# Performance work log

Measured on AMD Instinct MI355X. Metric: run time of the kernel, lower is better.

The kernel has to match this reference:

```python
import jax, jax.numpy as jnp
import numpy as np
from jax import lax

ANGRES = 5


def _conv(x, w, stride=(1, 1), pad=((1, 1), (1, 1)), dil=(1, 1)):
    return lax.conv_general_dilated(x, w, stride, pad, rhs_dilation=dil,
                                    dimension_numbers=('NCHW', 'OIHW', 'NCHW'))


def _lrelu(x):
    return jnp.where(x >= 0, x, 0.1 * x)


def _block_s(x, w):
    # SAI input: split into 5x5 grid of (sh,sw) views, conv each view, emit MacPI-interleaved layout
    B, C, H, W = x.shape
    sh, sw = H // 5, W // 5
    p = x.reshape(B, C, 5, sh, 5, sw).transpose(0, 2, 4, 1, 3, 5).reshape(B * 25, C, sh, sw)
    y = _conv(p, w).reshape(B, 5, 5, C, sh, sw)
    # (B,bi,bj,C,sh,sw) -> (B,C,sh,bi,sw,bj) -> (B,C,H,W)   [torch permute(0,3,4,1,5,2)]
    return y.transpose(0, 3, 4, 1, 5, 2).reshape(B, C, H, W)


def _block_a(x, w):
    # MacPI input: conv each 5x5 macropixel independently (zero pad at block edges)
    B, C, H, W = x.shape
    nh, nw = H // 5, W // 5
    p = x.reshape(B, C, nh, 5, nw, 5).transpose(0, 2, 4, 1, 3, 5).reshape(B * nh * nw, C, 5, 5)
    y = _conv(p, w)
    return y.reshape(B, nh, nw, C, 5, 5).transpose(0, 3, 1, 4, 2, 5).reshape(B, C, H, W)


def _epi(x, w1, w2, a):
    # EPI conv: [1,3a] kernel, stride [1,a], pad [0,a]; then 1x1 to a*C; then 1D pixel shuffle on W
    y = _lrelu(_conv(x, w1, stride=(1, a), pad=((0, 0), (a, a))))
    y = _lrelu(_conv(y, w2, pad=((0, 0), (0, 0))))
    B, aC, H, Wa = y.shape
    C = aC // a
    return y.reshape(B, a, C, H, Wa).transpose(0, 2, 3, 4, 1).reshape(B, C, H, Wa * a)


def _att_fuse(buf, alpha, gamma, beta, eps=1e-5):
    # covariance-based GLU attention over the N=4 branches
    B, NC, H, W = buf.shape
    N = 4
    C = NC // N
    x5 = buf.reshape(B, N, C, H, W)
    xr = x5.reshape(B, N, C * H * W)
    M = xr.shape[-1]
    xc = xr - jnp.mean(xr, axis=-1, keepdims=True)
    cov = jnp.einsum('bnm,bkm->bnk', xc, xc) * (alpha / (M - 1))  # [B,N,N]
    norm = cov / jnp.sqrt(jnp.mean(cov * cov, axis=(1, 2), keepdims=True) + eps)
    g = gamma * norm + beta
    att = g * jax.nn.sigmoid(g)  # GLU of duplicated halves
    out = jnp.einsum('bnk,bkm->bnm', att, xr).reshape(B, N, C, H, W) + x5
    return out.reshape(B, NC, H, W)


def _mac2sai(x, a):
    B, C, HU, WV = x.shape
    h, w = HU // a, WV // a
    return x.reshape(B, C, a, h, a, w).transpose(0, 1, 3, 5, 2, 4).reshape(B, C, h * a, w * a)


def _tsfefb(x, x1, ws, wa, we1, we2, al, ga, be, wf1, wf2, a):
    feaSpa = _lrelu(_block_s(x1, ws))
    feaAng = _lrelu(_block_a(x, wa))
    feaH = _epi(x, we1, we2, a)
    feaV = jnp.transpose(_epi(jnp.transpose(x, (0, 1, 3, 2)), we1, we2, a), (0, 1, 3, 2))
    buf = jnp.concatenate([feaSpa, feaAng, feaH, feaV], axis=1)
    out = _att_fuse(buf, al, ga, be)
    y = _lrelu(_conv(out, wf1, pad=((0, 0), (0, 0))))
    y = _conv(y, wf2, pad=((a, a), (a, a)), dil=(a, a))
    return y + x


def setup_inputs() -> dict:
    key = jax.random.key(0)
    ks = jax.random.split(key, 12)
    B, C, a, n = 4, 64, ANGRES, 4
    H = W = a * 32  # 160

    def w(k, shape):
        fan_in = float(np.prod(shape[2:]))
        return jax.random.normal(k, shape, jnp.float32) / np.float32(np.sqrt(fan_in))

    return {
        'x': jax.random.normal(ks[0], (B, C, H, W), jnp.float32),
        'x1': jax.random.normal(ks[1], (B, C, H, W), jnp.float32),
        'w_spa': w(ks[2], (n, C, C, 3, 3)),
        'w_ang': w(ks[3], (n, C, C, 3, 3)),
        'w_epi1': w(ks[4], (n, C, C, 1, 3 * a)),
        'w_epi2': w(ks[5], (n, a * C, C, 1, 1)),
        'alpha': jnp.ones((n,), jnp.float32),
        'gamma': 0.1 * jax.random.normal(ks[6], (n,), jnp.float32),
        'beta': 0.1 * jax.random.normal(ks[7], (n,), jnp.float32),
        'w_fuse1': w(ks[8], (n, C, 4 * C, 1, 1)),
        'w_fuse2': w(ks[9], (n, C, C, 3, 3)),
    }


def reference(x, x1, w_spa, w_ang, w_epi1, w_epi2, alpha, gamma, beta, w_fuse1, w_fuse2):
    a = ANGRES
    buf, buf1 = x, x1
    for i in range(w_spa.shape[0]):
        buf = _tsfefb(buf, buf1, w_spa[i], w_ang[i], w_epi1[i], w_epi2[i],
                      alpha[i], gamma[i], beta[i], w_fuse1[i], w_fuse2[i], a)
        buf1 = _mac2sai(buf, a)
    return buf
```

## Files before the change

### kernel.cpp

```cpp
#include <hip/hip_runtime.h>

__device__ __forceinline__ float lrelu(float v){ return v >= 0.f ? v : 0.1f*v; }


__global__ __launch_bounds__(256) void k_spa(const float* __restrict__ buf1, const float* __restrict__ w,
                                             float* __restrict__ out){
  const int b = blockIdx.x / 50, r2 = blockIdx.x % 50;
  const int view = r2 >> 1, half = r2 & 1;
  const int bi = view / 5, bj = view % 5;
  const int th0 = half*16;
  const int cog = blockIdx.y;
  const int tid = threadIdx.x;
  __shared__ float plane[2][18*38];
  for (int idx=tid; idx<2*18*38; idx+=256) ((float*)plane)[idx]=0.f;
  float acc[2][8];
  #pragma unroll
  for (int k=0;k<2;k++)
    #pragma unroll
    for (int c=0;c<8;c++) acc[k][c]=0.f;
  const float* src = buf1 + (size_t)b*1638400 + bi*32*160 + bj*32;
  const float* wb = w + (size_t)(cog*8)*576;
  const int sr = tid >> 3, sq = (tid & 7)*4;
  const int vr = th0 - 1 + sr;
  const bool rowok = (tid < 144) && ((unsigned)vr < 32u);
  __syncthreads();
  if (rowok)
    *(float4*)&plane[0][sr*38 + 4 + sq] = *(const float4*)(src + vr*160 + sq);
  __syncthreads();
  const int lr = tid >> 5, c = tid & 31;
  for (int ci=0; ci<64; ci++){
    float4 nx;
    const bool ld = rowok && (ci < 63);
    if (ld) nx = *(const float4*)(src + (size_t)(ci+1)*25600 + vr*160 + sq);
    const float* P = plane[ci & 1];
    float t0[9], t1[9];
    {
      const float* pp = &P[lr*38 + c + 3];
      t0[0]=pp[0];  t0[1]=pp[1];  t0[2]=pp[2];
      t0[3]=pp[38]; t0[4]=pp[39]; t0[5]=pp[40];
      t0[6]=pp[76]; t0[7]=pp[77]; t0[8]=pp[78];
      const float* qq = pp + 8*38;
      t1[0]=qq[0];  t1[1]=qq[1];  t1[2]=qq[2];
      t1[3]=qq[38]; t1[4]=qq[39]; t1[5]=qq[40];
      t1[6]=qq[76]; t1[7]=qq[77]; t1[8]=qq[78];
    }
    #pragma unroll
    for (int co=0;co<8;co++){
      const float* wp = wb + (size_t)co*576 + ci*9;
      float w0=wp[0],w1=wp[1],w2=wp[2],w3=wp[3],w4=wp[4],w5=wp[5],w6=wp[6],w7=wp[7],w8=wp[8];
      acc[0][co] += t0[0]*w0+t0[1]*w1+t0[2]*w2+t0[3]*w3+t0[4]*w4
                  + t0[5]*w5+t0[6]*w6+t0[7]*w7+t0[8]*w8;
      acc[1][co] += t1[0]*w0+t1[1]*w1+t1[2]*w2+t1[3]*w3+t1[4]*w4
                  + t1[5]*w5+t1[6]*w6+t1[7]*w7+t1[8]*w8;
    }
    if (ld) *(float4*)&plane[(ci+1)&1][sr*38 + 4 + sq] = nx;
    __syncthreads();
  }
  #pragma unroll
  for (int k=0;k<2;k++){
    int si = th0 + lr + k*8;
    int h = si*5 + bi, wq = c*5 + bj;
    #pragma unroll
    for (int co=0;co<8;co++){
      int ch = b*64 + cog*8 + co;
      out[(size_t)ch*25600 + h*160 + wq] = lrelu(acc[k][co]);
    }
  }
}

__global__ __launch_bounds__(320) void k_ang(const float* __restrict__ bufA, const float* __restrict__ w,
                                             float* __restrict__ out){
  const int b = blockIdx.x >> 4, mip = blockIdx.x & 15;
  const int cog = blockIdx.y;
  const int tid = threadIdx.x;
  __shared__ float lds[2][2240];
  for (int i=tid; i<2*2240; i+=320) ((float*)lds)[i] = 0.f;

  const int u = tid >> 6, mi_l = (tid >> 5) & 1, mp = tid & 31;
  int offm[3], offa[3];
  #pragma unroll
  for (int du=0; du<3; du++){
    offm[du] = mi_l*896 + (u+du)*128 + mp*4;
    offa[du] = 1792 + mi_l*224 + (u+du)*32 + mp;
  }
  const bool st1 = tid < 80;
  int sdst0[4], sdst1[4];
  const int rr0 = tid/40,       q0 = tid%40;
  const int rr1 = (tid+320)/40, q1 = (tid+320)%40;
  #pragma unroll
  for (int j=0;j<4;j++){
    int g = q0*4+j, mpw = g/5, vw = g - mpw*5;
    int miw = rr0/5, uw = rr0 - miw*5;
    sdst0[j] = (vw<4) ? (miw*896 + (1+uw)*128 + mpw*4 + vw)
                      : (1792 + miw*224 + (1+uw)*32 + mpw);
    g = q1*4+j; mpw = g/5; vw = g - mpw*5;
    miw = rr1/5; uw = rr1 - miw*5;
    sdst1[j] = (vw<4) ? (miw*896 + (1+uw)*128 + mpw*4 + vw)
                      : (1792 + miw*224 + (1+uw)*32 + mpw);
  }
  const float* src = bufA + (size_t)b*1638400 + (size_t)(mip*10)*160;
  const float* wb = w + (size_t)(cog*4)*576;

  float acc[4][5];
  #pragma unroll
  for (int co=0;co<4;co++)
    #pragma unroll
    for (int v=0;v<5;v++) acc[co][v]=0.f;

  __syncthreads();
  {
    float4 x0 = *(const float4*)(src + rr0*160 + q0*4);
    lds[0][sdst0[0]]=x0.x; lds[0][sdst0[1]]=x0.y; lds[0][sdst0[2]]=x0.z; lds[0][sdst0[3]]=x0.w;
    if (st1){
      float4 x1 = *(const float4*)(src + rr1*160 + q1*4);
      lds[0][sdst1[0]]=x1.x; lds[0][sdst1[1]]=x1.y; lds[0][sdst1[2]]=x1.z; lds[0][sdst1[3]]=x1.w;
    }
  }
  __syncthreads();
  for (int ci=0; ci<64; ci++){
    float4 n0, n1;
    if (ci < 63){
      n0 = *(const float4*)(src + (size_t)(ci+1)*25600 + rr0*160 + q0*4);
      if (st1) n1 = *(const float4*)(src + (size_t)(ci+1)*25600 + rr1*160 + q1*4);
    }
    const float* P = lds[ci & 1];
    float c[3][5];
    #pragma unroll
    for (int du=0;du<3;du++){
      float4 m = *(const float4*)&P[offm[du]];
      c[du][0]=m.x; c[du][1]=m.y; c[du][2]=m.z; c[du][3]=m.w;
      c[du][4]=P[offa[du]];
    }
    #pragma unroll
    for (int co=0;co<4;co++){
      const float* wp = wb + (size_t)co*576 + ci*9;
      float w0=wp[0],w1=wp[1],w2=wp[2],w3=wp[3],w4=wp[4],w5=wp[5],w6=wp[6],w7=wp[7],w8=wp[8];
      acc[co][0] += c[0][0]*w1 + c[0][1]*w2
                  + c[1][0]*w4 + c[1][1]*w5
                  + c[2][0]*w7 + c[2][1]*w8;
      acc[co][1] += c[0][0]*w0 + c[0][1]*w1 + c[0][2]*w2
                  + c[1][0]*w3 + c[1][1]*w4 + c[1][2]*w5
                  + c[2][0]*w6 + c[2][1]*w7 + c[2][2]*w8;
      acc[co][2] += c[0][1]*w0 + c[0][2]*w1 + c[0][3]*w2
                  + c[1][1]*w3 + c[1][2]*w4 + c[1][3]*w5
                  + c[2][1]*w6 + c[2][2]*w7 + c[2][3]*w8;
      acc[co][3] += c[0][2]*w0 + c[0][3]*w1 + c[0][4]*w2
                  + c[1][2]*w3 + c[1][3]*w4 + c[1][4]*w5
                  + c[2][2]*w6 + c[2][3]*w7 + c[2][4]*w8;
      acc[co][4] += c[0][3]*w0 + c[0][4]*w1
                  + c[1][3]*w3 + c[1][4]*w4
                  + c[2][3]*w6 + c[2][4]*w7;
    }
    if (ci < 63){
      float* Q = lds[(ci+1)&1];
      Q[sdst0[0]]=n0.x; Q[sdst0[1]]=n0.y; Q[sdst0[2]]=n0.z; Q[sdst0[3]]=n0.w;
      if (st1){ Q[sdst1[0]]=n1.x; Q[sdst1[1]]=n1.y; Q[sdst1[2]]=n1.z; Q[sdst1[3]]=n1.w; }
    }
    __syncthreads();
  }
  const int h = (mip*2 + mi_l)*5 + u;
  const int wc0 = mp*5;
  #pragma unroll
  for (int co=0;co<4;co++){
    int ch = b*64 + cog*4 + co;
    float* op = out + (size_t)ch*25600 + (size_t)h*160 + wc0;
    op[0]=lrelu(acc[co][0]); op[1]=lrelu(acc[co][1]); op[2]=lrelu(acc[co][2]);
    op[3]=lrelu(acc[co][3]); op[4]=lrelu(acc[co][4]);
  }
}

template<int VERT>
__global__ __launch_bounds__(320) void k_epi(const float* __restrict__ bufA, const float* __restrict__ we1,
                                             const float* __restrict__ we2, float* __restrict__ out){
  const int b = blockIdx.x / 160, hw = blockIdx.x % 160;
  const int tid = threadIdx.x;
  __shared__ float rowp[64*176];
  __shared__ float y1s[64*32];
  if (VERT){
    for (int idx=tid; idx<10240; idx+=320){
      int ci = idx/160, x = idx - ci*160;
      rowp[ci*176 + 8 + x] = bufA[(size_t)b*1638400 + (size_t)ci*25600 + (size_t)x*160 + hw];
    }
  } else {
    for (int ft=tid; ft<2560; ft+=320){
      int ci = ft/40, xq = (ft - ci*40)*4;
      *(float4*)&rowp[ci*176 + 8 + xq] =
        *(const float4*)(bufA + (size_t)b*1638400 + (size_t)ci*25600 + (size_t)hw*160 + xq);
    }
  }
  for (int idx=tid; idx<64*16; idx+=320){
    int ci = idx>>4, j = idx&15;
    rowp[ci*176 + (j<8 ? j : 160+j)] = 0.f;
  }
  __syncthreads();
  if (tid < 256){
    const int co = tid >> 2, wv0 = (tid & 3)*8;
    const int a0 = 2 + wv0*5;
    float acc[8];
    #pragma unroll
    for (int j=0;j<8;j++) acc[j]=0.f;
    const float* wp0 = we1 + (size_t)co*960;
    for (int ci=0; ci<64; ci++){
      float fl[52];
      const float* rp = &rowp[ci*176 + a0];
      #pragma unroll
      for (int m=0;m<26;m++) *(float2*)&fl[2*m] = *(const float2*)&rp[2*m];
      const float* wp = wp0 + ci*15;
      #pragma unroll
      for (int t=0;t<15;t++){
        float wt = wp[t];
        #pragma unroll
        for (int j=0;j<8;j++) acc[j] += fl[1 + j*5 + t]*wt;
      }
    }
    #pragma unroll
    for (int j=0;j<8;j++) y1s[co*32 + wv0 + j] = lrelu(acc[j]);
  }
  __syncthreads();
  {
    const int oc = tid, kk = oc >> 6, c = oc & 63;
    float a2[32];
    #pragma unroll
    for (int wv=0;wv<32;wv++) a2[wv]=0.f;
    const float* wp = we2 + (size_t)oc*64;
    for (int ci=0; ci<64; ci++){
      float wt = wp[ci];
      const float* yp = &y1s[ci*32];
      #pragma unroll
      for (int wv=0; wv<32; wv++) a2[wv] += yp[wv]*wt;
    }
    float* y2s = rowp;
    #pragma unroll
    for (int wv=0; wv<32; wv++) y2s[c*160 + wv*5 + kk] = lrelu(a2[wv]);
  }
  __syncthreads();
  {
    const float* y2s = rowp;
    for (int k=0;k<8;k++){
      int f = (tid + k*320)*4;
      int c = f/160, rr = f - c*160;
      *(float4*)(out + (size_t)(b*64+c)*25600 + (size_t)hw*160 + rr) = *(const float4*)&y2s[c*160+rr];
    }
  }
}

__global__ __launch_bounds__(256) void k_permV(const float* __restrict__ tmp, float* __restrict__ dst){
  const int bc = blockIdx.x;
  const int ti = blockIdx.y / 5, tj = blockIdx.y % 5;
  const int hw0 = ti*32, r0 = tj*32;
  const int lx = threadIdx.x & 31, ly = threadIdx.x >> 5;
  __shared__ float tile[32][33];
  const float* in = tmp + (size_t)bc*25600;
  float* outp = dst + (size_t)bc*25600;
  for (int yy=ly; yy<32; yy+=8)
    tile[yy][lx] = in[(size_t)(hw0+yy)*160 + r0 + lx];
  __syncthreads();
  for (int yy=ly; yy<32; yy+=8)
    outp[(size_t)(r0+yy)*160 + hw0 + lx] = tile[lx][yy];
}

__global__ __launch_bounds__(256) void k_permM(const float* __restrict__ A, float* __restrict__ dst){
  const int bc = blockIdx.x >> 5, hh = blockIdx.x & 31;
  const int tid = threadIdx.x;
  __shared__ float rows[5*160];
  const float* in = A + (size_t)bc*25600;
  if (tid < 200){
    int ai = tid/40, q = (tid - ai*40)*4;
    *(float4*)&rows[ai*160 + q] = *(const float4*)(in + (size_t)(ai*32+hh)*160 + q);
  }
  __syncthreads();
  float* outp = dst + (size_t)bc*25600 + (size_t)hh*800;
  for (int t=tid; t<800; t+=256){
    int ww = t/25, r2 = t - ww*25, ai = r2/5, aj = r2 - ai*5;
    outp[t] = rows[ai*160 + aj*32 + ww];
  }
}

__global__ __launch_bounds__(256) void k_red(const float* __restrict__ b0, const float* __restrict__ b1,
                                             const float* __restrict__ b2, const float* __restrict__ b3,
                                             float* __restrict__ part){
  const int b = blockIdx.y, blk = blockIdx.x;
  const int tid = threadIdx.x;
  const size_t off = (size_t)b*1638400 + (size_t)blk*25600;
  float s0=0,s1=0,s2=0,s3=0;
  float p00=0,p01=0,p02=0,p03=0,p11=0,p12=0,p13=0,p22=0,p23=0,p33=0;
  for (int it=0; it<25; it++){
    size_t m = off + it*1024 + tid*4;
    float4 x0 = *(const float4*)(b0+m);
    float4 x1 = *(const float4*)(b1+m);
    float4 x2 = *(const float4*)(b2+m);
    float4 x3 = *(const float4*)(b3+m);
    s0 += (x0.x+x0.y)+(x0.z+x0.w);
    s1 += (x1.x+x1.y)+(x1.z+x1.w);
    s2 += (x2.x+x2.y)+(x2.z+x2.w);
    s3 += (x3.x+x3.y)+(x3.z+x3.w);
    p00 += x0.x*x0.x+x0.y*x0.y+x0.z*x0.z+x0.w*x0.w;
    p01 += x0.x*x1.x+x0.y*x1.y+x0.z*x1.z+x0.w*x1.w;
    p02 += x0.x*x2.x+x0.y*x2.y+x0.z*x2.z+x0.w*x2.w;
    p03 += x0.x*x3.x+x0.y*x3.y+x0.z*x3.z+x0.w*x3.w;
    p11 += x1.x*x1.x+x1.y*x1.y+x1.z*x1.z+x1.w*x1.w;
    p12 += x1.x*x2.x+x1.y*x2.y+x1.z*x2.z+x1.w*x2.w;
    p13 += x1.x*x3.x+x1.y*x3.y+x1.z*x3.z+x1.w*x3.w;
    p22 += x2.x*x2.x+x2.y*x2.y+x2.z*x2.z+x2.w*x2.w;
    p23 += x2.x*x3.x+x2.y*x3.y+x2.z*x3.z+x2.w*x3.w;
    p33 += x3.x*x3.x+x3.y*x3.y+x3.z*x3.z+x3.w*x3.w;
  }
  float vals[14] = {s0,s1,s2,s3,p00,p01,p02,p03,p11,p12,p13,p22,p23,p33};
  __shared__ float red[4][14];
  int lane = tid & 63, wv = tid >> 6;
  #pragma unroll
  for (int j=0;j<14;j++){
    float v = vals[j];
    #pragma unroll
    for (int o=32;o>0;o>>=1) v += __shfl_down(v,o,64);
    if (lane==0) red[wv][j]=v;
  }
  __syncthreads();
  if (tid<14) part[((size_t)b*64+blk)*16 + tid] = red[0][tid]+red[1][tid]+red[2][tid]+red[3][tid];
}

__global__ __launch_bounds__(256) void k_attW(const float* __restrict__ part,
        const float* __restrict__ alpha, const float* __restrict__ gamma, const float* __restrict__ beta,
        int iblk, const float* __restrict__ wf1, float* __restrict__ Weff){
  const int b = blockIdx.x, tid = threadIdx.x;
  __shared__ float st[14];
  __shared__ float att[16];
  if (tid<14){
    float t=0;
    for (int blk=0;blk<64;blk++) t += part[((size_t)b*64+blk)*16 + tid];
    st[tid]=t;
  }
  __syncthreads();
  if (tid==0){
    const float M = 1638400.f;
    float s[4] = {st[0],st[1],st[2],st[3]};
    float S[4][4];
    S[0][0]=st[4];  S[0][1]=S[1][0]=st[5];  S[0][2]=S[2][0]=st[6];  S[0][3]=S[3][0]=st[7];
    S[1][1]=st[8];  S[1][2]=S[2][1]=st[9];  S[1][3]=S[3][1]=st[10];
    S[2][2]=st[11]; S[2][3]=S[3][2]=st[12]; S[3][3]=st[13];
    float al=alpha[iblk], ga=gamma[iblk], be=beta[iblk];
    float scale = al/(M-1.f);
    float cov[4][4], ss=0.f;
    for (int n=0;n<4;n++) for (int k=0;k<4;k++){
      float c = (S[n][k] - s[n]*s[k]/M)*scale;
      cov[n][k]=c; ss += c*c;
    }
    float rms = sqrtf(ss/16.f + 1e-5f);
    for (int n=0;n<4;n++) for (int k=0;k<4;k++){
      float g = ga*cov[n][k]/rms + be;
      att[n*4+k] = g/(1.f+expf(-g));
    }
  }
  __syncthreads();
  for (int idx=tid; idx<16384; idx+=256){
    int co=idx>>8, kc=idx&255, k=kc>>6, c=kc&63;
    float v = wf1[co*256+kc];
    #pragma unroll
    for (int n=0;n<4;n++) v += att[n*4+k]*wf1[co*256+n*64+c];
    Weff[(size_t)b*16384+idx] = v;
  }
}

__global__ __launch_bounds__(256) void k_fuse1(const float* b0, const float* __restrict__ b1,
                                               const float* __restrict__ b2, const float* __restrict__ b3,
                                               const float* __restrict__ Weff, float* y64){
  const int tile = blockIdx.x, b = blockIdx.y;
  const int px0 = tile*64;
  const int tid = threadIdx.x;
  const int ti = tid >> 4, tj = tid & 15;
  __shared__ float xs[64][68];
  __shared__ float wt[64][68];
  float acc[4][4];
  #pragma unroll
  for (int i=0;i<4;i++)
    #pragma unroll
    for (int j=0;j<4;j++) acc[i][j]=0.f;
  const float* bptr[4] = {b0,b1,b2,b3};
  for (int kb=0; kb<4; kb++){
    const float* xbk = bptr[kb] + (size_t)b*1638400 + px0;
    const float* wb = Weff + (size_t)b*16384 + kb*64;
    __syncthreads();
    for (int idx=tid; idx<4096; idx+=256){
      int kc=idx>>6, px=idx&63;
      xs[kc][px] = xbk[(size_t)kc*25600 + px];
    }
    for (int idx=tid; idx<4096; idx+=256){
      int co=idx>>6, k2=idx&63;
      wt[k2][co] = wb[co*256 + k2];
    }
    __syncthreads();
    for (int k2=0;k2<64;k2++){
      float4 a = *(const float4*)&wt[k2][ti*4];
      float4 v = *(const float4*)&xs[k2][tj*4];
      acc[0][0]+=a.x*v.x; acc[0][1]+=a.x*v.y; acc[0][2]+=a.x*v.z; acc[0][3]+=a.x*v.w;
      acc[1][0]+=a.y*v.x; acc[1][1]+=a.y*v.y; acc[1][2]+=a.y*v.z; acc[1][3]+=a.y*v.w;
      acc[2][0]+=a.z*v.x; acc[2][1]+=a.z*v.y; acc[2][2]+=a.z*v.z; acc[2][3]+=a.z*v.w;
      acc[3][0]+=a.w*v.x; acc[3][1]+=a.w*v.y; acc[3][2]+=a.w*v.z; acc[3][3]+=a.w*v.w;
    }
  }
  #pragma unroll
  for (int i=0;i<4;i++){
    int co = ti*4 + i;
    float4 o = make_float4(lrelu(acc[i][0]), lrelu(acc[i][1]), lrelu(acc[i][2]), lrelu(acc[i][3]));
    *(float4*)(y64 + ((size_t)(b*64+co))*25600 + px0 + tj*4) = o;
  }
}

template<int FINAL>
__global__ __launch_bounds__(256) void k_fuse2(const float* __restrict__ y64, const float* resid,
                                               const float* __restrict__ w, float* outp){
  const int b = blockIdx.x / 50, tile = blockIdx.x % 50;
  const int th0 = (tile/5)*16, tw0 = (tile%5)*32;
  const int cog = blockIdx.y;
  const int tid = threadIdx.x;
  __shared__ float plane[2][26*44];
  float acc[2][8];
  #pragma unroll
  for (int k=0;k<2;k++)
    #pragma unroll
    for (int c=0;c<8;c++) acc[k][c]=0.f;
  const float* src = y64 + (size_t)b*1638400;
  const float* wb = w + (size_t)(cog*8)*576;
  int soff[5], sdst[5];
  #pragma unroll
  for (int s=0;s<5;s++){
    int idx = tid + s*256;
    int r = idx/42, cc = idx - r*42;
    int gh = th0 + r - 5, gw = tw0 + cc - 5;
    sdst[s] = r*44 + cc;
    soff[s] = ((unsigned)gh < 160u && (unsigned)gw < 160u) ? (gh*160 + gw) : -1;
  }
  const bool s4 = (tid < 68);
  #pragma unroll
  for (int s=0;s<4;s++)
    plane[0][sdst[s]] = (soff[s] >= 0) ? src[soff[s]] : 0.f;
  if (s4) plane[0][sdst[4]] = (soff[4] >= 0) ? src[soff[4]] : 0.f;
  __syncthreads();
  const int lr = tid >> 5, c = tid & 31;
  for (int ci=0; ci<64; ci++){
    float nv[5];
    if (ci < 63){
      const float* s1 = src + (size_t)(ci+1)*25600;
      #pragma unroll
      for (int s=0;s<5;s++) nv[s] = (soff[s] >= 0) ? s1[soff[s]] : 0.f;
    }
    const float* P = plane[ci & 1];
    float t0[9], t1[9];
    {
      const float* pp = &P[lr*44 + c];
      t0[0]=pp[0];      t0[1]=pp[5];      t0[2]=pp[10];
      t0[3]=pp[220];    t0[4]=pp[225];    t0[5]=pp[230];
      t0[6]=pp[440];    t0[7]=pp[445];    t0[8]=pp[450];
      const float* qq = pp + 8*44;
      t1[0]=qq[0];      t1[1]=qq[5];      t1[2]=qq[10];
      t1[3]=qq[220];    t1[4]=qq[225];    t1[5]=qq[230];
      t1[6]=qq[440];    t1[7]=qq[445];    t1[8]=qq[450];
    }
    #pragma unroll
    for (int co=0;co<8;co++){
      const float* wp = wb + (size_t)co*576 + ci*9;
      float w0=wp[0],w1=wp[1],w2=wp[2],w3=wp[3],w4=wp[4],w5=wp[5],w6=wp[6],w7=wp[7],w8=wp[8];
      acc[0][co] += t0[0]*w0+t0[1]*w1+t0[2]*w2+t0[3]*w3+t0[4]*w4
                  + t0[5]*w5+t0[6]*w6+t0[7]*w7+t0[8]*w8;
      acc[1][co] += t1[0]*w0+t1[1]*w1+t1[2]*w2+t1[3]*w3+t1[4]*w4
                  + t1[5]*w5+t1[6]*w6+t1[7]*w7+t1[8]*w8;
    }
    if (ci < 63){
      float* Q = plane[(ci+1)&1];
      #pragma unroll
      for (int s=0;s<4;s++) Q[sdst[s]] = nv[s];
      if (s4) Q[sdst[4]] = nv[4];
    }
    __syncthreads();
  }
  #pragma unroll
  for (int k=0;k<2;k++){
    int h = th0 + lr + k*8, wq = tw0 + c;
    #pragma unroll
    for (int co=0;co<8;co++){
      int cg = cog*8 + co;
      size_t base = ((size_t)(b*64+cg)*160 + h)*160 + wq;
      outp[base] = acc[k][co] + resid[base];
    }
  }
}

extern "C" void kernel_launch(void* const* d_in, const int* in_sizes, int n_in,
                              void* d_out, int out_size, void* d_ws, size_t ws_size,
                              hipStream_t stream){
  const float* x    = (const float*)d_in[0];
  const float* x1   = (const float*)d_in[1];
  const float* wspa = (const float*)d_in[2];
  const float* wang = (const float*)d_in[3];
  const float* we1  = (const float*)d_in[4];
  const float* we2  = (const float*)d_in[5];
  const float* al   = (const float*)d_in[6];
  const float* ga   = (const float*)d_in[7];
  const float* be   = (const float*)d_in[8];
  const float* wf1  = (const float*)d_in[9];
  const float* wf2  = (const float*)d_in[10];

  char* ws = (char*)d_ws;
  const size_t SLOT = 26214400;
  float* A  = (float*)(ws);
  float* Bv = (float*)(ws +   SLOT);
  float* T1 = (float*)(ws + 2*SLOT);
  float* T2 = (float*)(ws + 3*SLOT);
  float* part = (float*)(ws + 4*SLOT);
  float* Weff = (float*)(ws + 4*SLOT + 16384);
  float* D = (float*)d_out;

  for (int i=0;i<4;i++){
    const float* Asrc  = (i==0) ? x  : (const float*)A;
    const float* B1src = (i==0) ? x1 : (const float*)Bv;
    k_epi<1><<<640,320,0,stream>>>(Asrc, we1 + (size_t)i*61440, we2 + (size_t)i*20480, T2);
    k_spa<<<dim3(200,8),256,0,stream>>>(B1src, wspa + (size_t)i*36864, T1);
    k_permV<<<dim3(256,25),256,0,stream>>>(T2, Bv);
    k_ang<<<dim3(64,16),320,0,stream>>>(Asrc, wang + (size_t)i*36864, T2);
    k_epi<0><<<640,320,0,stream>>>(Asrc, we1 + (size_t)i*61440, we2 + (size_t)i*20480, D);
    k_red<<<dim3(64,4),256,0,stream>>>(T1, T2, D, Bv, part);
    k_attW<<<4,256,0,stream>>>(part, al, ga, be, i, wf1 + (size_t)i*16384, Weff);
    k_fuse1<<<dim3(400,4),256,0,stream>>>(T1, T2, D, Bv, Weff, T1);
    if (i<3){
      k_fuse2<0><<<dim3(200,8),256,0,stream>>>(T1, Asrc, wf2 + (size_t)i*36864, A);
      k_permM<<<8192,256,0,stream>>>(A, Bv);
    } else {
      k_fuse2<1><<<dim3(200,8),256,0,stream>>>(T1, Asrc, wf2 + (size_t)i*36864, D);
    }
  }
}
```

Before: 3.108 ms.

## Transpose input before vertical EPI, swizzle conv block order for XCD locality, pad LDS

```diff
diff --git a/kernel.cpp b/kernel.cpp
--- a/kernel.cpp
+++ b/kernel.cpp
@@ -5,11 +5,13 @@
 
 __global__ __launch_bounds__(256) void k_spa(const float* __restrict__ buf1, const float* __restrict__ w,
                                              float* __restrict__ out){
-  const int b = blockIdx.x / 50, r2 = blockIdx.x % 50;
+  const int P = blockIdx.x;
+  const int within = P >> 3, cog = within & 7, tsel = within >> 3;
+  const int tg = (P & 7)*25 + tsel;
+  const int b = tg / 50, r2 = tg % 50;
   const int view = r2 >> 1, half = r2 & 1;
   const int bi = view / 5, bj = view % 5;
   const int th0 = half*16;
-  const int cog = blockIdx.y;
   const int tid = threadIdx.x;
   __shared__ float plane[2][18*38];
   for (int idx=tid; idx<2*18*38; idx+=256) ((float*)plane)[idx]=0.f;
@@ -32,10 +34,10 @@
     float4 nx;
     const bool ld = rowok && (ci < 63);
     if (ld) nx = *(const float4*)(src + (size_t)(ci+1)*25600 + vr*160 + sq);
-    const float* P = plane[ci & 1];
+    const float* P2 = plane[ci & 1];
     float t0[9], t1[9];
     {
-      const float* pp = &P[lr*38 + c + 3];
+      const float* pp = &P2[lr*38 + c + 3];
       t0[0]=pp[0];  t0[1]=pp[1];  t0[2]=pp[2];
       t0[3]=pp[38]; t0[4]=pp[39]; t0[5]=pp[40];
       t0[6]=pp[76]; t0[7]=pp[77]; t0[8]=pp[78];
@@ -70,8 +72,10 @@
 
 __global__ __launch_bounds__(320) void k_ang(const float* __restrict__ bufA, const float* __restrict__ w,
                                              float* __restrict__ out){
-  const int b = blockIdx.x >> 4, mip = blockIdx.x & 15;
-  const int cog = blockIdx.y;
+  const int P = blockIdx.x;
+  const int within = P >> 3, cog = within & 15, tsel = within >> 4;
+  const int tg = (P & 7)*8 + tsel;
+  const int b = tg >> 4, mip = tg & 15;
   const int tid = threadIdx.x;
   __shared__ float lds[2][2240];
   for (int i=tid; i<2*2240; i+=320) ((float*)lds)[i] = 0.f;
@@ -123,13 +127,13 @@
       n0 = *(const float4*)(src + (size_t)(ci+1)*25600 + rr0*160 + q0*4);
       if (st1) n1 = *(const float4*)(src + (size_t)(ci+1)*25600 + rr1*160 + q1*4);
     }
-    const float* P = lds[ci & 1];
+    const float* Pb = lds[ci & 1];
     float c[3][5];
     #pragma unroll
     for (int du=0;du<3;du++){
-      float4 m = *(const float4*)&P[offm[du]];
+      float4 m = *(const float4*)&Pb[offm[du]];
       c[du][0]=m.x; c[du][1]=m.y; c[du][2]=m.z; c[du][3]=m.w;
-      c[du][4]=P[offa[du]];
+      c[du][4]=Pb[offa[du]];
     }
     #pragma unroll
     for (int co=0;co<4;co++){
@@ -169,24 +173,16 @@
   }
 }
 
-template<int VERT>
 __global__ __launch_bounds__(320) void k_epi(const float* __restrict__ bufA, const float* __restrict__ we1,
                                              const float* __restrict__ we2, float* __restrict__ out){
   const int b = blockIdx.x / 160, hw = blockIdx.x % 160;
   const int tid = threadIdx.x;
   __shared__ float rowp[64*176];
   __shared__ float y1s[64*32];
-  if (VERT){
-    for (int idx=tid; idx<10240; idx+=320){
-      int ci = idx/160, x = idx - ci*160;
-      rowp[ci*176 + 8 + x] = bufA[(size_t)b*1638400 + (size_t)ci*25600 + (size_t)x*160 + hw];
-    }
-  } else {
-    for (int ft=tid; ft<2560; ft+=320){
-      int ci = ft/40, xq = (ft - ci*40)*4;
-      *(float4*)&rowp[ci*176 + 8 + xq] =
-        *(const float4*)(bufA + (size_t)b*1638400 + (size_t)ci*25600 + (size_t)hw*160 + xq);
-    }
+  for (int ft=tid; ft<2560; ft+=320){
+    int ci = ft/40, xq = (ft - ci*40)*4;
+    *(float4*)&rowp[ci*176 + 8 + xq] =
+      *(const float4*)(bufA + (size_t)b*1638400 + (size_t)ci*25600 + (size_t)hw*160 + xq);
   }
   for (int idx=tid; idx<64*16; idx+=320){
     int ci = idx>>4, j = idx&15;
@@ -231,7 +227,7 @@
     }
     float* y2s = rowp;
     #pragma unroll
-    for (int wv=0; wv<32; wv++) y2s[c*160 + wv*5 + kk] = lrelu(a2[wv]);
+    for (int wv=0; wv<32; wv++) y2s[c*164 + wv*5 + kk] = lrelu(a2[wv]);
   }
   __syncthreads();
   {
@@ -239,7 +235,7 @@
     for (int k=0;k<8;k++){
       int f = (tid + k*320)*4;
       int c = f/160, rr = f - c*160;
-      *(float4*)(out + (size_t)(b*64+c)*25600 + (size_t)hw*160 + rr) = *(const float4*)&y2s[c*160+rr];
+      *(float4*)(out + (size_t)(b*64+c)*25600 + (size_t)hw*160 + rr) = *(const float4*)&y2s[c*164+rr];
     }
   }
 }
@@ -409,9 +405,11 @@
 template<int FINAL>
 __global__ __launch_bounds__(256) void k_fuse2(const float* __restrict__ y64, const float* resid,
                                                const float* __restrict__ w, float* outp){
-  const int b = blockIdx.x / 50, tile = blockIdx.x % 50;
+  const int P = blockIdx.x;
+  const int within = P >> 3, cog = within & 7, tsel = within >> 3;
+  const int tg = (P & 7)*25 + tsel;
+  const int b = tg / 50, tile = tg % 50;
   const int th0 = (tile/5)*16, tw0 = (tile%5)*32;
-  const int cog = blockIdx.y;
   const int tid = threadIdx.x;
   __shared__ float plane[2][26*44];
   float acc[2][8];
@@ -444,10 +442,10 @@
       #pragma unroll
       for (int s=0;s<5;s++) nv[s] = (soff[s] >= 0) ? s1[soff[s]] : 0.f;
     }
-    const float* P = plane[ci & 1];
+    const float* Pb = plane[ci & 1];
     float t0[9], t1[9];
     {
-      const float* pp = &P[lr*44 + c];
+      const float* pp = &Pb[lr*44 + c];
       t0[0]=pp[0];      t0[1]=pp[5];      t0[2]=pp[10];
       t0[3]=pp[220];    t0[4]=pp[225];    t0[5]=pp[230];
       t0[6]=pp[440];    t0[7]=pp[445];    t0[8]=pp[450];
@@ -513,19 +511,20 @@
   for (int i=0;i<4;i++){
     const float* Asrc  = (i==0) ? x  : (const float*)A;
     const float* B1src = (i==0) ? x1 : (const float*)Bv;
-    k_epi<1><<<640,320,0,stream>>>(Asrc, we1 + (size_t)i*61440, we2 + (size_t)i*20480, T2);
-    k_spa<<<dim3(200,8),256,0,stream>>>(B1src, wspa + (size_t)i*36864, T1);
+    k_permV<<<dim3(256,25),256,0,stream>>>(Asrc, D);
+    k_epi<<<640,320,0,stream>>>(D, we1 + (size_t)i*61440, we2 + (size_t)i*20480, T2);
+    k_spa<<<1600,256,0,stream>>>(B1src, wspa + (size_t)i*36864, T1);
     k_permV<<<dim3(256,25),256,0,stream>>>(T2, Bv);
-    k_ang<<<dim3(64,16),320,0,stream>>>(Asrc, wang + (size_t)i*36864, T2);
-    k_epi<0><<<640,320,0,stream>>>(Asrc, we1 + (size_t)i*61440, we2 + (size_t)i*20480, D);
+    k_ang<<<1024,320,0,stream>>>(Asrc, wang + (size_t)i*36864, T2);
+    k_epi<<<640,320,0,stream>>>(Asrc, we1 + (size_t)i*61440, we2 + (size_t)i*20480, D);
     k_red<<<dim3(64,4),256,0,stream>>>(T1, T2, D, Bv, part);
     k_attW<<<4,256,0,stream>>>(part, al, ga, be, i, wf1 + (size_t)i*16384, Weff);
     k_fuse1<<<dim3(400,4),256,0,stream>>>(T1, T2, D, Bv, Weff, T1);
     if (i<3){
-      k_fuse2<0><<<dim3(200,8),256,0,stream>>>(T1, Asrc, wf2 + (size_t)i*36864, A);
+      k_fuse2<0><<<1600,256,0,stream>>>(T1, Asrc, wf2 + (size_t)i*36864, A);
       k_permM<<<8192,256,0,stream>>>(A, Bv);
     } else {
-      k_fuse2<1><<<dim3(200,8),256,0,stream>>>(T1, Asrc, wf2 + (size_t)i*36864, D);
-    }
-  }
-}
+      k_fuse2<1><<<1600,256,0,stream>>>(T1, Asrc, wf2 + (size_t)i*36864, D);
+    }
+  }
+}
```

Measured after the change: 2.912 ms. 6.3% less time.
